# Optimization experiments

Measured on AMD Instinct MI355X. Metric: run time of the kernel, lower is better.

Reference implementation:

```python
import jax, jax.numpy as jnp
import numpy as np

B, CIN, COUT, H, W, K = 4, 64, 64, 128, 128, 3
KK = K * K


def setup_inputs() -> dict:
    key = jax.random.key(0)
    k = jax.random.split(key, 7)
    return {
        "input_feat": jax.random.normal(k[0], (B, CIN, H, W), jnp.float32),
        "inter": jax.random.normal(k[1], (B, CIN, H, W), jnp.float32),
        "fea": jax.random.normal(k[2], (B, 4 * CIN, 1, 1), jnp.float32),
        "weight": jax.random.uniform(k[3], (COUT, CIN, K, K), jnp.float32, -1.0, 1.0) / np.float32(np.sqrt(CIN * KK)),
        "bias": jnp.zeros((COUT,), jnp.float32),
        # conv_offset_mask params (torch zero-inits; small random values used so offsets/masks are non-trivial)
        "com_w": jax.random.normal(k[4], (3 * KK, CIN, K, K), jnp.float32) * 0.01,
        "com_b": jnp.zeros((3 * KK,), jnp.float32),
        "c1_w": jax.random.normal(k[5], (COUT, 4 * CIN), jnp.float32) / np.float32(np.sqrt(4 * CIN)),
        "c2_w": jax.random.normal(k[6], (COUT, COUT), jnp.float32) / np.float32(np.sqrt(COUT)),
    }


def reference(input_feat, inter, fea, weight, bias, com_w, com_b, c1_w, c2_w):
    b, c, h, w = input_feat.shape
    # offset/mask prediction: 3x3 conv, stride 1, pad 1 -> [b, 3*KK, h, w]
    om = jax.lax.conv_general_dilated(inter, com_w, (1, 1), ((1, 1), (1, 1)),
                                      dimension_numbers=("NCHW", "OIHW", "NCHW"))
    om = om + com_b[None, :, None, None]
    offset = jnp.concatenate([om[:, :KK], om[:, KK:2 * KK]], axis=1)  # [b, 2*KK, h, w]
    mask = jax.nn.sigmoid(om[:, 2 * KK:])                              # [b, KK, h, w]
    dy, dx = offset[:, 0::2], offset[:, 1::2]                          # mmcv interleaved (y, x) per tap

    # dynamic per-sample weight modulation (Cout == Cin, fea scales the in-channel axis)
    fvec = jnp.einsum('oc,bc->bo', c1_w, fea[:, :, 0, 0])              # [b, COUT]
    wdyn = weight[None] * fvec[:, None, :, None, None]                 # [b, COUT, CIN, K, K]

    # sampling coordinates: base grid (stride=1, pad=1, dil=1) + learned offsets
    ky = jnp.repeat(jnp.arange(K), K).astype(jnp.float32)              # [KK]
    kx = jnp.tile(jnp.arange(K), K).astype(jnp.float32)
    base_y = jnp.arange(h, dtype=jnp.float32)[None, :, None] - 1.0 + ky[:, None, None]  # [KK, h, 1]
    base_x = jnp.arange(w, dtype=jnp.float32)[None, None, :] - 1.0 + kx[:, None, None]  # [KK, 1, w]
    ys = base_y[None] + dy                                             # [b, KK, h, w]
    xs = base_x[None] + dx

    y0f = jnp.floor(ys); x0f = jnp.floor(xs)
    ly = ys - y0f; lx = xs - x0f
    y0 = y0f.astype(jnp.int32); x0 = x0f.astype(jnp.int32)
    xf = input_feat.reshape(b, c, h * w)

    def gather(yi, xi, wgt):
        valid = (yi >= 0) & (yi < h) & (xi >= 0) & (xi < w)
        idx = jnp.clip(yi, 0, h - 1) * w + jnp.clip(xi, 0, w - 1)      # [b, KK, h, w]
        v = jnp.take_along_axis(xf, idx.reshape(b, 1, -1), axis=2).reshape(b, c, KK, h, w)
        return v * (wgt * valid)[:, None]

    val = (gather(y0, x0, (1 - ly) * (1 - lx)) + gather(y0, x0 + 1, (1 - ly) * lx)
           + gather(y0 + 1, x0, ly * (1 - lx)) + gather(y0 + 1, x0 + 1, ly * lx))
    val = val * mask[:, None]                                          # modulated samples [b, c, KK, h, w]

    out = jnp.einsum('bocp,bcphw->bohw', wdyn.reshape(b, COUT, c, KK), val) + bias[None, :, None, None]
    return jnp.einsum('oc,bchw->bohw', c2_w, out)                      # c2: 1x1 conv, no bias
```

## Files before the change

kernel.cpp:

```cpp
#include <hip/hip_runtime.h>
#include <math.h>

#define BB 4
#define CIN 64
#define COUT 64
#define HH 128
#define WW 128
#define HW (HH*WW)

typedef __attribute__((ext_vector_type(8))) short short8;
typedef __attribute__((ext_vector_type(4))) float f32x4;
typedef __attribute__((ext_vector_type(2))) float f32x2;
typedef __attribute__((ext_vector_type(4))) unsigned int uint4v;

static __device__ __forceinline__ unsigned short f2bf(float f) {
    unsigned int u = __builtin_bit_cast(unsigned int, f);
    u += 0x7fffu + ((u >> 16) & 1u);
    return (unsigned short)(u >> 16);
}
static __device__ __forceinline__ float bf2f(unsigned short h) {
    unsigned int u = ((unsigned int)h) << 16;
    return __builtin_bit_cast(float, u);
}
static __device__ __forceinline__ unsigned int cvtpk_bf16(float lo, float hi) {
    unsigned int r;
    asm("v_cvt_pk_bf16_f32 %0, %1, %2" : "=v"(r) : "v"(lo), "v"(hi));
    return r;
}
static __device__ __forceinline__ f32x2 bfpair(unsigned int u) {
    f32x2 r;
    r[0] = __builtin_bit_cast(float, u << 16);
    r[1] = __builtin_bit_cast(float, u & 0xffff0000u);
    return r;
}

__global__ __launch_bounds__(256) void prep_kernel(
        const float* __restrict__ com_w, const float* __restrict__ c2w,
        const float* __restrict__ bias,
        unsigned short* __restrict__ wk2, float* __restrict__ bias2) {
    int id = blockIdx.x, tid = threadIdx.x;
    if (id < 80) {
        int i = id*256 + tid;
        int k = i & 31, oc = (i >> 5) & 31;
        int cc5 = i >> 10;
        int cg = cc5 / 5, ch = cc5 % 5;
        int tap = ch*2 + (k >> 4);
        int c = cg*16 + (k & 15);
        float v = 0.f;
        if (tap < 9 && oc < 27) v = com_w[((size_t)oc*64 + c)*9 + tap];
        wk2[i] = f2bf(v);
    } else if (tid < COUT) {
        float s2 = 0.f;
        for (int o = 0; o < COUT; ++o) s2 += c2w[tid*COUT + o] * bias[o];
        bias2[tid] = s2;
    }
}

static __device__ __forceinline__ void transpose_body(
        const float* __restrict__ srcb, unsigned short* __restrict__ dstb,
        int tb, int tid, float* lt ) {
    int b = tb >> 8;
    int px0 = (tb & 255) * 64;
    const float* src = srcb + (size_t)b*CIN*HW + px0;
    for (int i = tid; i < 4096; i += 256) {
        int c = i >> 6, px = i & 63;
        lt[c*65 + px] = src[(size_t)c*HW + px];
    }
    __syncthreads();
    int q = tid & 3, px = tid >> 2;
    unsigned short* dst = dstb + ((size_t)b*HW + px0 + px)*64 + q*16;
    #pragma unroll
    for (int s = 0; s < 2; ++s) {
        short8 pk;
        #pragma unroll
        for (int j = 0; j < 8; ++j)
            pk[j] = (short)f2bf(lt[(q*16 + s*8 + j)*65 + px]);
        *(short8*)(dst + s*8) = pk;
    }
}

static __device__ __forceinline__ void w2_body(
        int wid, int tid, const float* __restrict__ weight,
        const float* __restrict__ c2w, const float* __restrict__ c1w,
        const float* __restrict__ fea,
        unsigned short* __restrict__ w2b, float* c2s, float* wcol) {
    int o2 = tid & 63, ci = tid >> 6;
    int lane = tid & 63;
    int bp = wid >> 4;
    int c_base = (wid & 15)*4;
    int p = bp % 9, b = bp / 9;
    int c = c_base + ci;

    float part = 0.f;
    #pragma unroll
    for (int s = 0; s < 4; ++s)
        part += c1w[c*(4*CIN) + lane + s*64] * fea[b*(4*CIN) + lane + s*64];
    #pragma unroll
    for (int off = 32; off; off >>= 1) part += __shfl_down(part, off);
    float fv = __shfl(part, 0);

    for (int idx = tid; idx < 4096; idx += 256) {
        int o2r = idx >> 6, oc = idx & 63;
        c2s[oc*65 + o2r] = c2w[idx];
    }
    {
        int o = tid & 63, cw = tid >> 6;
        wcol[cw*64 + o] = weight[(o*CIN + (c_base + cw))*9 + p];
    }
    __syncthreads();
    float s = 0.f;
    #pragma unroll 8
    for (int o = 0; o < COUT; ++o) s += c2s[o*65 + o2] * wcol[ci*64 + o];
    w2b[(size_t)bp*4096 + o2*64 + c] = f2bf(s * fv);
}

static __device__ __forceinline__ void conv_lds_body(
        int id, int tid, const float* __restrict__ inter,
        const unsigned short* __restrict__ wk2, const float* __restrict__ com_b,
        float* __restrict__ om, float* smemf) {
    unsigned short* til = (unsigned short*)smemf;
    int b  = id >> 7;
    int t7 = id & 127;
    int by = t7 >> 3;
    int bx = t7 & 7;
    int x0 = bx*16, y0 = by*8;
    int lane = tid & 63, wv = tid >> 6;
    int nn = lane & 15, qq = lane >> 4;

    if (tid < 24) til[180*24 + tid] = 0;

    int scl = tid & 15, scc = tid >> 4;
    int sgx  = x0 + scc - 1;
    int sgxc = max(sgx, 0);
    float sfx = ((unsigned)sgx < WW) ? 1.f : 0.f;

    f32x4 acc[2][2];
    #pragma unroll
    for (int nt = 0; nt < 2; ++nt)
        #pragma unroll
        for (int mh = 0; mh < 2; ++mh)
            #pragma unroll
            for (int j = 0; j < 4; ++j) acc[nt][mh][j] = 0.f;

    for (int cg = 0; cg < 4; ++cg) {
        __syncthreads();
        const float* I = inter + ((size_t)(b*CIN + cg*16))*HW;

        {
            const float* colp = I + (size_t)scl*HW + sgxc;
            unsigned short* tp = til + scc*24 + scl;
            #pragma unroll
            for (int r = 0; r < 10; ++r) {
                int gy  = y0 + r - 1;
                int gyc = min(max(gy, 0), HH-1);
                float m = ((unsigned)gy < HH) ? sfx : 0.f;
                float v = colp[(size_t)gyc*WW] * m;
                tp[r*(18*24)] = f2bf(v);
            }
        }
        #pragma unroll
        for (int k = 0; k < 2; ++k) {
            int i = k*256 + tid;
            if (i < 320) {
                int cl  = i & 15;
                int ccb = (i >> 4) & 1;
                int r   = i >> 5;
                int gx  = x0 + 15 + ccb;
                int gy  = y0 + r - 1;
                int gxc = min(gx, WW-1);
                int gyc = min(max(gy, 0), HH-1);
                float m = (((unsigned)gy < HH) && ((unsigned)gx < WW)) ? 1.f : 0.f;
                float v = I[(size_t)cl*HW + gyc*WW + gxc] * m;
                til[(r*18 + 16 + ccb)*24 + cl] = f2bf(v);
            }
        }
        __syncthreads();

        #pragma unroll
        for (int ch = 0; ch < 5; ++ch) {
            short8 a0 = *(const short8*)(wk2 +
                (((size_t)(cg*5 + ch)*32 + nn)*32 + qq*8));
            short8 a1 = *(const short8*)(wk2 +
                (((size_t)(cg*5 + ch)*32 + 16 + nn)*32 + qq*8));
            int tap = ch*2 + (qq >> 1);
            #pragma unroll
            for (int nt = 0; nt < 2; ++nt) {
                int row = wv*2 + nt;
                int px_idx;
                if (tap > 8) px_idx = 180;
                else {
                    int ky = tap/3, kx = tap%3;
                    px_idx = (row + ky)*18 + (nn + kx);
                }
                short8 bfr = *(const short8*)(til + px_idx*24 + (qq&1)*8);
                acc[nt][0] = __builtin_amdgcn_mfma_f32_16x16x32_bf16(
                                 a0, bfr, acc[nt][0], 0, 0, 0);
                acc[nt][1] = __builtin_amdgcn_mfma_f32_16x16x32_bf16(
                                 a1, bfr, acc[nt][1], 0, 0, 0);
            }
        }
    }

    float* op = om + (size_t)b*27*HW;
    #pragma unroll
    for (int nt = 0; nt < 2; ++nt) {
        int pix = (y0 + wv*2 + nt)*WW + x0 + nn;
        #pragma unroll
        for (int mh = 0; mh < 2; ++mh)
            #pragma unroll
            for (int j = 0; j < 4; ++j) {
                int oc = mh*16 + qq*4 + j;
                if (oc < 27)
                    op[(size_t)oc*HW + pix] = acc[nt][mh][j] + com_b[oc];
            }
    }
}

__global__ __launch_bounds__(256) void main2_kernel(
        const float* __restrict__ input_feat,
        const float* __restrict__ inter,
        const unsigned short* __restrict__ wk2,
        const float* __restrict__ com_b,
        const float* __restrict__ weight,
        const float* __restrict__ c2w,
        const float* __restrict__ c1w,
        const float* __restrict__ fea,
        float* __restrict__ om, unsigned short* __restrict__ w2b,
        unsigned short* __restrict__ fT) {
    __shared__ __align__(16) float smem[4416];
    int id = blockIdx.x, tid = threadIdx.x;
    if (id < 512)        conv_lds_body(id, tid, inter, wk2, com_b, om, smem);
    else if (id < 1088)  w2_body(id - 512, tid, weight, c2w, c1w, fea, w2b,
                                 smem, smem + 64*65);
    else                 transpose_body(input_feat, fT, id - 1088, tid, smem);
}

__global__ __launch_bounds__(256) void dcn_main_kernel(
        const unsigned short* __restrict__ fT,
        const unsigned short* __restrict__ w2b,
        const float* __restrict__ bias2,
        const float* __restrict__ om,
        float* __restrict__ out) {
    int id = blockIdx.x;
    int xcd = id & 7;
    int b   = xcd >> 1;
    int xh  = xcd & 1;
    int y   = id >> 3;

    int t = threadIdx.x;
    int lane = t & 63, wv = t >> 6;
    int nn = lane & 15, qq = lane >> 4;
    int px0 = xh*64 + wv*16;
    int x = px0 + nn;
    int pix = y*WW + x;
    const unsigned short* Fb = fT + (size_t)b*HW*64;
    const float* omb = om + (size_t)b*27*HW;
    const unsigned short* w2p = w2b + (size_t)(b*9)*4096 + qq*8;
    int co = qq*8;

    f32x4 acc[4];
    #pragma unroll
    for (int mt = 0; mt < 4; ++mt)
        #pragma unroll
        for (int j = 0; j < 4; ++j)
            acc[mt][j] = bias2[mt*16 + qq*4 + j];

    float omy = omb[pix];
    float omx = omb[(size_t)HW + pix];
    float omm = omb[(size_t)18*HW + pix];

    #pragma unroll
    for (int p = 0; p < 9; ++p) {
        short8 afrL[4], afrH[4];
        #pragma unroll
        for (int mt = 0; mt < 4; ++mt) {
            const unsigned short* ap = w2p + (size_t)p*4096 + (mt*16 + nn)*64;
            afrL[mt] = *(const short8*)(ap);
            afrH[mt] = *(const short8*)(ap + 32);
        }

        float mv = 1.f / (1.f + expf(-omm));
        float ysv = (float)(y - 1 + p/3) + omy;
        float xsv = (float)(x - 1 + p%3) + omx;
        float y0f = floorf(ysv), x0f = floorf(xsv);
        float ly = ysv - y0f, lx = xsv - x0f;
        int y0 = (int)y0f, x0i = (int)x0f;
        int y1 = y0 + 1, x1 = x0i + 1;
        float vy0 = (y0 >= 0 && y0 < HH) ? 1.f : 0.f;
        float vy1 = (y1 >= 0 && y1 < HH) ? 1.f : 0.f;
        float vx0 = (x0i >= 0 && x0i < WW) ? 1.f : 0.f;
        float vx1 = (x1 >= 0 && x1 < WW) ? 1.f : 0.f;
        float w00 = (1.f-ly)*(1.f-lx)*mv * vy0*vx0;
        float w01 = (1.f-ly)*lx      *mv * vy0*vx1;
        float w10 = ly      *(1.f-lx)*mv * vy1*vx0;
        float w11 = ly      *lx      *mv * vy1*vx1;
        int y0c = min(max(y0,0),HH-1), y1c = min(max(y1,0),HH-1);
        int x0c = min(max(x0i,0),WW-1), x1c = min(max(x1,0),WW-1);
        int i00 = y0c*WW + x0c, i01 = y0c*WW + x1c;
        int i10 = y1c*WW + x0c, i11 = y1c*WW + x1c;

        if (p < 8) {
            omy = omb[(size_t)(2*p+2)*HW + pix];
            omx = omb[(size_t)(2*p+3)*HW + pix];
            omm = omb[(size_t)(19+p )*HW + pix];
        }

        const unsigned short* p00 = Fb + (size_t)i00*64 + co;
        const unsigned short* p01 = Fb + (size_t)i01*64 + co;
        const unsigned short* p10 = Fb + (size_t)i10*64 + co;
        const unsigned short* p11 = Fb + (size_t)i11*64 + co;
        short8 c00L = *(const short8*)(p00);
        short8 c01L = *(const short8*)(p01);
        short8 c10L = *(const short8*)(p10);
        short8 c11L = *(const short8*)(p11);
        short8 c00H = *(const short8*)(p00 + 32);
        short8 c01H = *(const short8*)(p01 + 32);
        short8 c10H = *(const short8*)(p10 + 32);
        short8 c11H = *(const short8*)(p11 + 32);

        uint4v u00 = __builtin_bit_cast(uint4v, c00L);
        uint4v u01 = __builtin_bit_cast(uint4v, c01L);
        uint4v u10 = __builtin_bit_cast(uint4v, c10L);
        uint4v u11 = __builtin_bit_cast(uint4v, c11L);
        unsigned int pw[4];
        #pragma unroll
        for (int jp = 0; jp < 4; ++jp) {
            f32x2 A = bfpair(u00[jp]);
            f32x2 B = bfpair(u01[jp]);
            f32x2 C = bfpair(u10[jp]);
            f32x2 D = bfpair(u11[jp]);
            f32x2 r = A*w00 + B*w01 + C*w10 + D*w11;
            pw[jp] = cvtpk_bf16(r[0], r[1]);
        }
        uint4v u4L = {pw[0], pw[1], pw[2], pw[3]};
        short8 bfrL = __builtin_bit_cast(short8, u4L);
        #pragma unroll
        for (int mt = 0; mt < 4; ++mt)
            acc[mt] = __builtin_amdgcn_mfma_f32_16x16x32_bf16(
                          afrL[mt], bfrL, acc[mt], 0, 0, 0);

        u00 = __builtin_bit_cast(uint4v, c00H);
        u01 = __builtin_bit_cast(uint4v, c01H);
        u10 = __builtin_bit_cast(uint4v, c10H);
        u11 = __builtin_bit_cast(uint4v, c11H);
        #pragma unroll
        for (int jp = 0; jp < 4; ++jp) {
            f32x2 A = bfpair(u00[jp]);
            f32x2 B = bfpair(u01[jp]);
            f32x2 C = bfpair(u10[jp]);
            f32x2 D = bfpair(u11[jp]);
            f32x2 r = A*w00 + B*w01 + C*w10 + D*w11;
            pw[jp] = cvtpk_bf16(r[0], r[1]);
        }
        uint4v u4H = {pw[0], pw[1], pw[2], pw[3]};
        short8 bfrH = __builtin_bit_cast(short8, u4H);
        #pragma unroll
        for (int mt = 0; mt < 4; ++mt)
            acc[mt] = __builtin_amdgcn_mfma_f32_16x16x32_bf16(
                          afrH[mt], bfrH, acc[mt], 0, 0, 0);
    }

    float* outp = out + (size_t)b*COUT*HW + (size_t)y*WW + px0 + nn;
    #pragma unroll
    for (int mt = 0; mt < 4; ++mt)
        #pragma unroll
        for (int j = 0; j < 4; ++j)
            outp[(size_t)(mt*16 + qq*4 + j)*HW] = acc[mt][j];
}

extern "C" void kernel_launch(void* const* d_in, const int* in_sizes, int n_in,
                              void* d_out, int out_size, void* d_ws, size_t ws_size,
                              hipStream_t stream) {
    const float* input_feat = (const float*)d_in[0];
    const float* inter      = (const float*)d_in[1];
    const float* fea        = (const float*)d_in[2];
    const float* weight     = (const float*)d_in[3];
    const float* bias       = (const float*)d_in[4];
    const float* com_w      = (const float*)d_in[5];
    const float* com_b      = (const float*)d_in[6];
    const float* c1w        = (const float*)d_in[7];
    const float* c2w        = (const float*)d_in[8];
    float* out = (float*)d_out;

    float* ws    = (float*)d_ws;
    float* bias2 = ws + 256;
    unsigned short* w2b = (unsigned short*)(ws + 512);
    float* om    = ws + 512 + 73728;
    unsigned short* wk2 = (unsigned short*)(om + 1769472);
    unsigned short* fT  = wk2 + 20480;

    prep_kernel<<<81, 256, 0, stream>>>(com_w, c2w, bias, wk2, bias2);
    main2_kernel<<<2112, 256, 0, stream>>>(input_feat, inter, wk2, com_b,
                                           weight, c2w, c1w, fea, om, w2b, fT);
    dcn_main_kernel<<<1024, 256, 0, stream>>>(fT, w2b, bias2, om, out);
}
```

Measured before the change: 177.8 us.

## Stage a swizzled input-feature halo tile in LDS for deformable bilinear gathers

Each block of the DCN main kernel now covers a 32-pixel row segment with 128 threads instead of 64 pixels with 256, and first loads a 5x36-pixel, 64-channel bf16 halo tile of the transposed features into XOR-swizzled shared memory. Bilinear corner reads whose coordinates fall inside the tile are served from LDS. Reads that fall outside it go back to global memory. The aim is to replace scattered global gathers with LDS reads, since small offsets keep most samples within a 2-pixel halo. The cost is a prologue load plus a barrier per block, twice as many blocks, and a divergent fallback path when offsets are large.

Result: faster. 163.4 us (-8.1%).

```diff
diff --git a/kernel.cpp b/kernel.cpp
--- a/kernel.cpp
+++ b/kernel.cpp
@@ -235,28 +235,50 @@
     else                 transpose_body(input_feat, fT, id - 1088, tid, smem);
 }
 
-__global__ __launch_bounds__(256) void dcn_main_kernel(
+__global__ __launch_bounds__(128, 4) void dcn_main_kernel(
         const unsigned short* __restrict__ fT,
         const unsigned short* __restrict__ w2b,
         const float* __restrict__ bias2,
         const float* __restrict__ om,
         float* __restrict__ out) {
+    __shared__ __align__(16) unsigned short gtile[5*36*64];
     int id = blockIdx.x;
     int xcd = id & 7;
+    int jj  = id >> 3;
     int b   = xcd >> 1;
-    int xh  = xcd & 1;
-    int y   = id >> 3;
+    int y   = jj & 127;
+    int xq  = ((xcd & 1) << 1) | (jj >> 7);
 
     int t = threadIdx.x;
     int lane = t & 63, wv = t >> 6;
     int nn = lane & 15, qq = lane >> 4;
-    int px0 = xh*64 + wv*16;
+    int px0 = xq*32 + wv*16;
     int x = px0 + nn;
     int pix = y*WW + x;
     const unsigned short* Fb = fT + (size_t)b*HW*64;
     const float* omb = om + (size_t)b*27*HW;
     const unsigned short* w2p = w2b + (size_t)(b*9)*4096 + qq*8;
-    int co = qq*8;
+    int co  = qq*8;
+    int cob = qq*16;
+
+    int ybase = min(max(y - 2, 0), HH - 5);
+    int xbase = min(max(xq*32 - 2, 0), WW - 36);
+
+    char* gt = (char*)gtile;
+    #pragma unroll
+    for (int it = 0; it < 12; ++it) {
+        int c = it*128 + t;
+        if (c < 1440) {
+            int pl = c >> 3;
+            int ci = c & 7;
+            int sy = (pl*1821) >> 16;
+            int sx = pl - sy*36;
+            short8 v = *(const short8*)(Fb +
+                ((size_t)(ybase + sy)*WW + xbase + sx)*64 + ci*8);
+            int bo = (pl*128 + ci*16) ^ ((pl & 7) << 4);
+            *(short8*)(gt + bo) = v;
+        }
+    }
 
     f32x4 acc[4];
     #pragma unroll
@@ -268,6 +290,7 @@
     float omy = omb[pix];
     float omx = omb[(size_t)HW + pix];
     float omm = omb[(size_t)18*HW + pix];
+    __syncthreads();
 
     #pragma unroll
     for (int p = 0; p < 9; ++p) {
@@ -296,8 +319,6 @@
         float w11 = ly      *lx      *mv * vy1*vx1;
         int y0c = min(max(y0,0),HH-1), y1c = min(max(y1,0),HH-1);
         int x0c = min(max(x0i,0),WW-1), x1c = min(max(x1,0),WW-1);
-        int i00 = y0c*WW + x0c, i01 = y0c*WW + x1c;
-        int i10 = y1c*WW + x0c, i11 = y1c*WW + x1c;
 
         if (p < 8) {
             omy = omb[(size_t)(2*p+2)*HW + pix];
@@ -305,18 +326,44 @@
             omm = omb[(size_t)(19+p )*HW + pix];
         }
 
-        const unsigned short* p00 = Fb + (size_t)i00*64 + co;
-        const unsigned short* p01 = Fb + (size_t)i01*64 + co;
-        const unsigned short* p10 = Fb + (size_t)i10*64 + co;
-        const unsigned short* p11 = Fb + (size_t)i11*64 + co;
-        short8 c00L = *(const short8*)(p00);
-        short8 c01L = *(const short8*)(p01);
-        short8 c10L = *(const short8*)(p10);
-        short8 c11L = *(const short8*)(p11);
-        short8 c00H = *(const short8*)(p00 + 32);
-        short8 c01H = *(const short8*)(p01 + 32);
-        short8 c10H = *(const short8*)(p10 + 32);
-        short8 c11H = *(const short8*)(p11 + 32);
+        short8 c00L, c01L, c10L, c11L, c00H, c01H, c10H, c11H;
+        {
+            int sy0 = y0c - ybase, sy1 = y1c - ybase;
+            int sx0 = x0c - xbase, sx1 = x1c - xbase;
+            bool allin = ((unsigned)sy0 < 5) & ((unsigned)sy1 < 5) &
+                         ((unsigned)sx0 < 36) & ((unsigned)sx1 < 36);
+            if (allin) {
+                int p00 = sy0*36 + sx0, p01 = sy0*36 + sx1;
+                int p10 = sy1*36 + sx0, p11 = sy1*36 + sx1;
+                int o00 = (p00*128 + cob) ^ ((p00&7)<<4);
+                int o01 = (p01*128 + cob) ^ ((p01&7)<<4);
+                int o10 = (p10*128 + cob) ^ ((p10&7)<<4);
+                int o11 = (p11*128 + cob) ^ ((p11&7)<<4);
+                c00L = *(const short8*)(gt + o00);
+                c01L = *(const short8*)(gt + o01);
+                c10L = *(const short8*)(gt + o10);
+                c11L = *(const short8*)(gt + o11);
+                c00H = *(const short8*)(gt + (o00 ^ 64));
+                c01H = *(const short8*)(gt + (o01 ^ 64));
+                c10H = *(const short8*)(gt + (o10 ^ 64));
+                c11H = *(const short8*)(gt + (o11 ^ 64));
+            } else {
+                int i00 = y0c*WW + x0c, i01 = y0c*WW + x1c;
+                int i10 = y1c*WW + x0c, i11 = y1c*WW + x1c;
+                const unsigned short* g00 = Fb + (size_t)i00*64 + co;
+                const unsigned short* g01 = Fb + (size_t)i01*64 + co;
+                const unsigned short* g10 = Fb + (size_t)i10*64 + co;
+                const unsigned short* g11 = Fb + (size_t)i11*64 + co;
+                c00L = *(const short8*)(g00);
+                c01L = *(const short8*)(g01);
+                c10L = *(const short8*)(g10);
+                c11L = *(const short8*)(g11);
+                c00H = *(const short8*)(g00 + 32);
+                c01H = *(const short8*)(g01 + 32);
+                c10H = *(const short8*)(g10 + 32);
+                c11H = *(const short8*)(g11 + 32);
+            }
+        }
 
         uint4v u00 = __builtin_bit_cast(uint4v, c00L);
         uint4v u01 = __builtin_bit_cast(uint4v, c01L);
@@ -392,5 +439,5 @@
     prep_kernel<<<81, 256, 0, stream>>>(com_w, c2w, bias, wk2, bias2);
     main2_kernel<<<2112, 256, 0, stream>>>(input_feat, inter, wk2, com_b,
                                            weight, c2w, c1w, fea, om, w2b, fT);
-    dcn_main_kernel<<<1024, 256, 0, stream>>>(fT, w2b, bias2, om, out);
-}
+    dcn_main_kernel<<<2048, 128, 0, stream>>>(fT, w2b, bias2, om, out);
+}
```
